# Kernel optimization log

Measured on AMD Instinct MI355X. Metric: run time of the kernel, lower is better.

The kernel has to match this reference:

```python
import jax, jax.numpy as jnp
from jax import lax
import numpy as np

B, T, IN, H, NC = 2048, 512, 1, 128, 8


def setup_inputs() -> dict:
    key = jax.random.key(0)
    ks = jax.random.split(key, 13)
    s = 0.05
    inp = {
        "x": jax.random.normal(ks[0], (B, T, IN), dtype=jnp.float32),
        # layer 0 LSTM params (PyTorch layout: W_ih [4H, in], W_hh [4H, H])
        "W_ih0": jax.random.normal(ks[1], (4 * H, IN), dtype=jnp.float32) * s,
        "W_hh0": jax.random.normal(ks[2], (4 * H, H), dtype=jnp.float32) * s,
        "b_ih0": jax.random.normal(ks[3], (4 * H,), dtype=jnp.float32) * s,
        "b_hh0": jax.random.normal(ks[4], (4 * H,), dtype=jnp.float32) * s,
        # layer 1 LSTM params
        "W_ih1": jax.random.normal(ks[5], (4 * H, H), dtype=jnp.float32) * s,
        "W_hh1": jax.random.normal(ks[6], (4 * H, H), dtype=jnp.float32) * s,
        "b_ih1": jax.random.normal(ks[7], (4 * H,), dtype=jnp.float32) * s,
        "b_hh1": jax.random.normal(ks[8], (4 * H,), dtype=jnp.float32) * s,
        # classifier: Linear(H,64) -> ReLU -> Linear(64,NC)
        "W1": jax.random.normal(ks[9], (64, H), dtype=jnp.float32) * s,
        "b1": jax.random.normal(ks[10], (64,), dtype=jnp.float32) * s,
        "W2": jax.random.normal(ks[11], (NC, 64), dtype=jnp.float32) * s,
        "b2": jax.random.normal(ks[12], (NC,), dtype=jnp.float32) * s,
    }
    return inp


def _lstm_layer(x_seq, W_ih, W_hh, b_ih, b_hh):
    # x_seq: [B, T, in]. PyTorch gate order: i, f, g, o.
    bsz = x_seq.shape[0]
    h_dim = W_hh.shape[1]
    # Precompute input projections for all timesteps (big GEMM outside scan).
    x_proj = jnp.einsum('bti,gi->btg', x_seq, W_ih) + b_ih + b_hh  # [B, T, 4H]

    def step(carry, xp_t):
        h, c = carry
        gates = xp_t + h @ W_hh.T  # [B, 4H]
        i_g, f_g, g_g, o_g = jnp.split(gates, 4, axis=-1)
        i_g = jax.nn.sigmoid(i_g)
        f_g = jax.nn.sigmoid(f_g)
        g_g = jnp.tanh(g_g)
        o_g = jax.nn.sigmoid(o_g)
        c = f_g * c + i_g * g_g
        h = o_g * jnp.tanh(c)
        return (h, c), h

    init = (jnp.zeros((bsz, h_dim), x_seq.dtype), jnp.zeros((bsz, h_dim), x_seq.dtype))
    (_, _), hs = lax.scan(step, init, jnp.swapaxes(x_proj, 0, 1))  # hs: [T, B, H]
    return jnp.swapaxes(hs, 0, 1)  # [B, T, H]


def reference(x, W_ih0, W_hh0, b_ih0, b_hh0, W_ih1, W_hh1, b_ih1, b_hh1, W1, b1, W2, b2):
    h0 = _lstm_layer(x, W_ih0, W_hh0, b_ih0, b_hh0)   # [B, T, H]
    h1 = _lstm_layer(h0, W_ih1, W_hh1, b_ih1, b_hh1)  # [B, T, H] (dropout off in eval)
    last = h1[:, -1, :]                                # [B, H]
    hidden = jax.nn.relu(last @ W1.T + b1)             # [B, 64]
    logits = hidden @ W2.T + b2                        # [B, NC]
    return logits
```

## Files before the change

kernel.cpp:

```cpp
#include <hip/hip_runtime.h>
#include <stdint.h>

typedef float f32x4 __attribute__((ext_vector_type(4)));
typedef short s16x8 __attribute__((ext_vector_type(8)));
typedef short s16x4 __attribute__((ext_vector_type(4)));
typedef uint32_t u32x4 __attribute__((ext_vector_type(4)));

#define HDIM 128
#define TLEN 512
#define BT 16

__device__ __forceinline__ unsigned short f2bf(float f) {
    union { float f; uint32_t u; } v; v.f = f;
    uint32_t r = v.u + 0x7FFFu + ((v.u >> 16) & 1u);
    return (unsigned short)(r >> 16);
}
__device__ __forceinline__ float bfhi(uint32_t u){ union{uint32_t u;float f;}v; v.u = u & 0xFFFF0000u; return v.f; }
__device__ __forceinline__ float bflo(uint32_t u){ union{uint32_t u;float f;}v; v.u = u << 16; return v.f; }
__device__ __forceinline__ float bf2f(short s){ union{uint32_t u;float f;}v; v.u = ((uint32_t)(unsigned short)s) << 16; return v.f; }

__device__ __forceinline__ float sigmoidf_(float x){
    float e = __expf(-x);
    return __builtin_amdgcn_rcpf(1.0f + e);
}
__device__ __forceinline__ float tanhf_(float x){
    float e = __expf(2.0f * x);
    return 1.0f - 2.0f * __builtin_amdgcn_rcpf(1.0f + e);
}

#define MFMA16(A, B, C) __builtin_amdgcn_mfma_f32_16x16x32_bf16((A), (B), (C), 0, 0, 0)

__global__ __launch_bounds__(512, 2) void lstm_fused_kernel(
    const float* __restrict__ x,
    const float* __restrict__ Wih0,
    const float* __restrict__ Whh0,
    const float* __restrict__ bih0,
    const float* __restrict__ bhh0,
    const float* __restrict__ Wih1,
    const float* __restrict__ Whh1,
    const float* __restrict__ bih1,
    const float* __restrict__ bhh1,
    const float* __restrict__ W1,
    const float* __restrict__ b1,
    const float* __restrict__ W2,
    const float* __restrict__ b2,
    float* __restrict__ out)
{
    __shared__ __align__(16) short wh1lds[65536];
    __shared__ __align__(16) short h0f0[2048], h0f1[2048];
    __shared__ __align__(16) short h1f0[2048], h1f1[2048];
    __shared__ __align__(16) float b1lds[4][8][16];

    const int tid = threadIdx.x;
    const int w   = tid >> 6;
    const int wl  = w & 3;
    const bool isL0 = (w < 4);
    const int l = tid & 63;
    const int n = l & 15;
    const int q = l >> 4;
    const int b0 = blockIdx.x * BT;
    const float* xrow = x + (size_t)(b0 + n) * TLEN;

    for (int s2 = tid; s2 < 8192; s2 += 512) {
        const int ll = s2 & 63, t2 = (s2 >> 6) & 7, cc = (s2 >> 9) & 3, wv = s2 >> 11;
        const int row = (t2 >> 1) * 128 + 32 * wv + 16 * (t2 & 1) + (ll & 15);
        const int k0  = cc * 32 + (ll >> 4) * 8;
        const float* p = Whh1 + row * HDIM + k0;
        s16x8 a;
        #pragma unroll
        for (int j = 0; j < 8; ++j) a[j] = (short)f2bf(p[j]);
        *(s16x8*)&wh1lds[s2 * 8] = a;
    }
    {
        const int idx = tid;
        const int wv = idx >> 7, t2 = (idx >> 4) & 7, j = idx & 15;
        const int row = (t2 >> 1) * 128 + 32 * wv + 16 * (t2 & 1) + j;
        b1lds[wv][t2][j] = bih1[row] + bhh1[row];
    }
    for (int s2 = tid; s2 < 1024; s2 += 512) ((uint32_t*)h1f1)[s2] = 0u;

    const int ub0 = 32 * wl + 4 * q;
    const int ub1 = ub0 + 16;
    const int fo0 = ((ub0 >> 5) * 64 + n + 16 * ((ub0 >> 3) & 3)) * 8 + (ub0 & 7);
    const int fo1 = ((ub1 >> 5) * 64 + n + 16 * ((ub1 >> 3) & 3)) * 8 + (ub1 & 7);

#define L0ITER(K, R0, W0) do {                                                \
    const int xi_ = (K) + 1;                                                  \
    const float xv_ = xrow[xi_ < TLEN ? xi_ : (TLEN - 1)];                    \
    s16x8 hb_[4];                                                             \
    _Pragma("unroll")                                                         \
    for (int c = 0; c < 4; ++c) hb_[c] = *(const s16x8*)&(R0)[(c * 64 + l) * 8]; \
    f32x4 a_[8];                                                              \
    _Pragma("unroll")                                                         \
    for (int t2 = 0; t2 < 8; ++t2) {                                          \
        _Pragma("unroll")                                                     \
        for (int r = 0; r < 4; ++r)                                           \
            a_[t2][r] = fmaf(bfhi(bwx[t2][r]), xv_, bflo(bwx[t2][r]));        \
    }                                                                         \
    _Pragma("unroll")                                                         \
    for (int c = 0; c < 4; ++c) {                                             \
        _Pragma("unroll")                                                     \
        for (int t2 = 0; t2 < 8; ++t2)                                        \
            a_[t2] = MFMA16(w0f[c][t2], hb_[c], a_[t2]);                      \
    }                                                                         \
    _Pragma("unroll")                                                         \
    for (int h = 0; h < 2; ++h) {                                             \
        s16x4 hw;                                                             \
        _Pragma("unroll")                                                     \
        for (int r = 0; r < 4; ++r) {                                         \
            const float ig = sigmoidf_(a_[0 + h][r]);                         \
            const float fg = sigmoidf_(a_[2 + h][r]);                         \
            const float gg = tanhf_(a_[4 + h][r]);                            \
            const float og = sigmoidf_(a_[6 + h][r]);                         \
            const float cc = fmaf(fg, c0_[h][r], ig * gg);                    \
            c0_[h][r] = cc;                                                   \
            hw[r] = (short)f2bf(og * tanhf_(cc));                             \
        }                                                                     \
        *(s16x4*)&(W0)[h ? fo1 : fo0] = hw;                                   \
    }                                                                         \
    __syncthreads();                                                          \
} while (0)

#define L1ITER(K, R0, R1, W1) do {                                            \
    s16x8 hb0_[4], hb1_[4];                                                   \
    _Pragma("unroll")                                                         \
    for (int c = 0; c < 4; ++c) {                                             \
        hb0_[c] = *(const s16x8*)&(R0)[(c * 64 + l) * 8];                     \
        hb1_[c] = *(const s16x8*)&(R1)[(c * 64 + l) * 8];                     \
    }                                                                         \
    f32x4 a_[8];                                                              \
    _Pragma("unroll")                                                         \
    for (int t2 = 0; t2 < 8; ++t2)                                            \
        a_[t2] = *(const f32x4*)&b1lds[wl][t2][q * 4];                        \
    _Pragma("unroll")                                                         \
    for (int c = 0; c < 4; ++c) {                                             \
        _Pragma("unroll")                                                     \
        for (int t2 = 0; t2 < 8; ++t2)                                        \
            a_[t2] = MFMA16(wi1f[c][t2], hb0_[c], a_[t2]);                    \
    }                                                                         \
    _Pragma("unroll")                                                         \
    for (int c = 0; c < 4; ++c) {                                             \
        s16x8 wt_[8];                                                         \
        _Pragma("unroll")                                                     \
        for (int t2 = 0; t2 < 8; ++t2)                                        \
            wt_[t2] = *(const s16x8*)&wh1lds[(((wl * 4 + c) * 8 + t2) * 64 + l) * 8]; \
        _Pragma("unroll")                                                     \
        for (int t2 = 0; t2 < 8; ++t2)                                        \
            a_[t2] = MFMA16(wt_[t2], hb1_[c], a_[t2]);                        \
    }                                                                         \
    _Pragma("unroll")                                                         \
    for (int h = 0; h < 2; ++h) {                                             \
        s16x4 hw;                                                             \
        _Pragma("unroll")                                                     \
        for (int r = 0; r < 4; ++r) {                                         \
            const float ig = sigmoidf_(a_[0 + h][r]);                         \
            const float fg = sigmoidf_(a_[2 + h][r]);                         \
            const float gg = tanhf_(a_[4 + h][r]);                            \
            const float og = sigmoidf_(a_[6 + h][r]);                         \
            const float cc = fmaf(fg, c1_[h][r], ig * gg);                    \
            c1_[h][r] = cc;                                                   \
            hw[r] = (short)f2bf(og * tanhf_(cc));                             \
        }                                                                     \
        *(s16x4*)&(W1)[h ? fo1 : fo0] = hw;                                   \
    }                                                                         \
    __syncthreads();                                                          \
} while (0)

    if (isL0) {
        s16x8 w0f[4][8];
        #pragma unroll
        for (int c = 0; c < 4; ++c) {
            #pragma unroll
            for (int t2 = 0; t2 < 8; ++t2) {
                const int row = (t2 >> 1) * 128 + 32 * wl + 16 * (t2 & 1) + n;
                const int k0 = c * 32 + q * 8;
                const float* p = Whh0 + row * HDIM + k0;
                s16x8 a;
                #pragma unroll
                for (int j = 0; j < 8; ++j) a[j] = (short)f2bf(p[j]);
                w0f[c][t2] = a;
            }
        }
        u32x4 bwx[8];
        #pragma unroll
        for (int t2 = 0; t2 < 8; ++t2) {
            #pragma unroll
            for (int r = 0; r < 4; ++r) {
                const int row = (t2 >> 1) * 128 + 32 * wl + 16 * (t2 & 1) + 4 * q + r;
                bwx[t2][r] = ((uint32_t)f2bf(Wih0[row]) << 16) | f2bf(bih0[row] + bhh0[row]);
            }
        }
        float c0_[2][4] = {{0.f,0.f,0.f,0.f},{0.f,0.f,0.f,0.f}};

        {
            const float x0 = xrow[0];
            #pragma unroll
            for (int h = 0; h < 2; ++h) {
                s16x4 hw;
                #pragma unroll
                for (int r = 0; r < 4; ++r) {
                    const float pi = fmaf(bfhi(bwx[0 + h][r]), x0, bflo(bwx[0 + h][r]));
                    const float pg = fmaf(bfhi(bwx[4 + h][r]), x0, bflo(bwx[4 + h][r]));
                    const float po = fmaf(bfhi(bwx[6 + h][r]), x0, bflo(bwx[6 + h][r]));
                    const float ig = sigmoidf_(pi);
                    const float gg = tanhf_(pg);
                    const float og = sigmoidf_(po);
                    const float cc = ig * gg;
                    c0_[h][r] = cc;
                    hw[r] = (short)f2bf(og * tanhf_(cc));
                }
                *(s16x4*)&h0f0[h ? fo1 : fo0] = hw;
            }
        }
        __syncthreads();

        #pragma unroll 1
        for (int k = 0; k < TLEN; k += 2) {
            L0ITER(k,     h0f0, h0f1);
            L0ITER(k + 1, h0f1, h0f0);
        }
    } else {
        s16x8 wi1f[4][8];
        #pragma unroll
        for (int c = 0; c < 4; ++c) {
            #pragma unroll
            for (int t2 = 0; t2 < 8; ++t2) {
                const int row = (t2 >> 1) * 128 + 32 * wl + 16 * (t2 & 1) + n;
                const int k0 = c * 32 + q * 8;
                const float* p = Wih1 + row * HDIM + k0;
                s16x8 a;
                #pragma unroll
                for (int j = 0; j < 8; ++j) a[j] = (short)f2bf(p[j]);
                wi1f[c][t2] = a;
            }
        }
        float c1_[2][4] = {{0.f,0.f,0.f,0.f},{0.f,0.f,0.f,0.f}};

        __syncthreads();

        #pragma unroll 1
        for (int k = 0; k < TLEN; k += 2) {
            L1ITER(k,     h0f0, h1f1, h1f0);
            L1ITER(k + 1, h0f1, h1f0, h1f1);
        }
    }

    float* headH = (float*)wh1lds;
    float* headL = headH + 16 * HDIM;
    if (!isL0) {
        #pragma unroll
        for (int h = 0; h < 2; ++h) {
            const s16x4 hv = *(const s16x4*)&h1f1[h ? fo1 : fo0];
            f32x4 hf;
            #pragma unroll
            for (int r = 0; r < 4; ++r) hf[r] = bf2f(hv[r]);
            *(f32x4*)&headH[n * HDIM + (h ? ub1 : ub0)] = hf;
        }
    }
    __syncthreads();

    #pragma unroll
    for (int rep = 0; rep < 2; ++rep) {
        const int idx = tid + rep * 512;
        const int nn = idx >> 6, j = idx & 63;
        float s = b1[j];
        const float* wrow = W1 + j * HDIM;
        const float* hrow = headH + nn * HDIM;
        #pragma unroll
        for (int k = 0; k < HDIM; k += 4) {
            const f32x4 hv = *(const f32x4*)&hrow[k];
            const f32x4 wv = *(const f32x4*)&wrow[k];
            s += hv[0]*wv[0] + hv[1]*wv[1] + hv[2]*wv[2] + hv[3]*wv[3];
        }
        headL[nn * 64 + j] = fmaxf(s, 0.0f);
    }
    __syncthreads();

    if (tid < 128) {
        const int nn = tid >> 3, cls = tid & 7;
        float s = b2[cls];
        const float* wrow = W2 + cls * 64;
        const float* hrow = headL + nn * 64;
        #pragma unroll
        for (int k = 0; k < 64; k += 4) {
            const f32x4 hv = *(const f32x4*)&hrow[k];
            const f32x4 wv = *(const f32x4*)&wrow[k];
            s += hv[0]*wv[0] + hv[1]*wv[1] + hv[2]*wv[2] + hv[3]*wv[3];
        }
        out[(size_t)(b0 + nn) * 8 + cls] = s;
    }
}

extern "C" void kernel_launch(void* const* d_in, const int* in_sizes, int n_in,
                              void* d_out, int out_size, void* d_ws, size_t ws_size,
                              hipStream_t stream) {
    const float* x    = (const float*)d_in[0];
    const float* Wih0 = (const float*)d_in[1];
    const float* Whh0 = (const float*)d_in[2];
    const float* bih0 = (const float*)d_in[3];
    const float* bhh0 = (const float*)d_in[4];
    const float* Wih1 = (const float*)d_in[5];
    const float* Whh1 = (const float*)d_in[6];
    const float* bih1 = (const float*)d_in[7];
    const float* bhh1 = (const float*)d_in[8];
    const float* W1   = (const float*)d_in[9];
    const float* b1   = (const float*)d_in[10];
    const float* W2   = (const float*)d_in[11];
    const float* b2   = (const float*)d_in[12];
    float* outp = (float*)d_out;

    lstm_fused_kernel<<<128, 512, 0, stream>>>(
        x, Wih0, Whh0, bih0, bhh0, Wih1, Whh1, bih1, bhh1, W1, b1, W2, b2, outp);
}
```

Before: 954.4 us.

## Replace block barriers with LDS counter flags and 4-deep h0 ring buffer

The per-timestep __syncthreads between layer-0 and layer-1 wavegroups is replaced by LDS atomic counters that each wave polls with s_sleep. A 4-slot ring buffer for layer-0 hidden states lets layer 0 run up to two steps ahead of layer 1, so the two layers no longer stall in lockstep. The last layer-1 step is peeled out and writes fp32 h directly to the head buffer. The cost is spin-wait polling overhead and fragile memory-ordering assumptions around the LDS flags.

```diff
diff --git a/kernel.cpp b/kernel.cpp
--- a/kernel.cpp
+++ b/kernel.cpp
@@ -47,9 +47,10 @@
     float* __restrict__ out)
 {
     __shared__ __align__(16) short wh1lds[65536];
-    __shared__ __align__(16) short h0f0[2048], h0f1[2048];
-    __shared__ __align__(16) short h1f0[2048], h1f1[2048];
+    __shared__ __align__(16) short h0ring[4][2048];
+    __shared__ __align__(16) short h1f[2][2048];
     __shared__ __align__(16) float b1lds[4][8][16];
+    __shared__ int syncc[2];
 
     const int tid = threadIdx.x;
     const int w   = tid >> 6;
@@ -61,6 +62,8 @@
     const int b0 = blockIdx.x * BT;
     const float* xrow = x + (size_t)(b0 + n) * TLEN;
 
+    if (tid == 0) { syncc[0] = 0; syncc[1] = 0; }
+
     for (int s2 = tid; s2 < 8192; s2 += 512) {
         const int ll = s2 & 63, t2 = (s2 >> 6) & 7, cc = (s2 >> 9) & 3, wv = s2 >> 11;
         const int row = (t2 >> 1) * 128 + 32 * wv + 16 * (t2 & 1) + (ll & 15);
@@ -77,93 +80,23 @@
         const int row = (t2 >> 1) * 128 + 32 * wv + 16 * (t2 & 1) + j;
         b1lds[wv][t2][j] = bih1[row] + bhh1[row];
     }
-    for (int s2 = tid; s2 < 1024; s2 += 512) ((uint32_t*)h1f1)[s2] = 0u;
+    for (int s2 = tid; s2 < 1024; s2 += 512) ((uint32_t*)h1f[1])[s2] = 0u;
 
     const int ub0 = 32 * wl + 4 * q;
     const int ub1 = ub0 + 16;
     const int fo0 = ((ub0 >> 5) * 64 + n + 16 * ((ub0 >> 3) & 3)) * 8 + (ub0 & 7);
     const int fo1 = ((ub1 >> 5) * 64 + n + 16 * ((ub1 >> 3) & 3)) * 8 + (ub1 & 7);
 
-#define L0ITER(K, R0, W0) do {                                                \
-    const int xi_ = (K) + 1;                                                  \
-    const float xv_ = xrow[xi_ < TLEN ? xi_ : (TLEN - 1)];                    \
-    s16x8 hb_[4];                                                             \
-    _Pragma("unroll")                                                         \
-    for (int c = 0; c < 4; ++c) hb_[c] = *(const s16x8*)&(R0)[(c * 64 + l) * 8]; \
-    f32x4 a_[8];                                                              \
-    _Pragma("unroll")                                                         \
-    for (int t2 = 0; t2 < 8; ++t2) {                                          \
-        _Pragma("unroll")                                                     \
-        for (int r = 0; r < 4; ++r)                                           \
-            a_[t2][r] = fmaf(bfhi(bwx[t2][r]), xv_, bflo(bwx[t2][r]));        \
-    }                                                                         \
-    _Pragma("unroll")                                                         \
-    for (int c = 0; c < 4; ++c) {                                             \
-        _Pragma("unroll")                                                     \
-        for (int t2 = 0; t2 < 8; ++t2)                                        \
-            a_[t2] = MFMA16(w0f[c][t2], hb_[c], a_[t2]);                      \
-    }                                                                         \
-    _Pragma("unroll")                                                         \
-    for (int h = 0; h < 2; ++h) {                                             \
-        s16x4 hw;                                                             \
-        _Pragma("unroll")                                                     \
-        for (int r = 0; r < 4; ++r) {                                         \
-            const float ig = sigmoidf_(a_[0 + h][r]);                         \
-            const float fg = sigmoidf_(a_[2 + h][r]);                         \
-            const float gg = tanhf_(a_[4 + h][r]);                            \
-            const float og = sigmoidf_(a_[6 + h][r]);                         \
-            const float cc = fmaf(fg, c0_[h][r], ig * gg);                    \
-            c0_[h][r] = cc;                                                   \
-            hw[r] = (short)f2bf(og * tanhf_(cc));                             \
-        }                                                                     \
-        *(s16x4*)&(W0)[h ? fo1 : fo0] = hw;                                   \
-    }                                                                         \
-    __syncthreads();                                                          \
+#define WAITGE(T0, T1) do {                                                   \
+    volatile const int* f0_ = &syncc[0];                                      \
+    volatile const int* f1_ = &syncc[1];                                      \
+    while (*f0_ < (T0) || *f1_ < (T1)) __builtin_amdgcn_s_sleep(1);           \
+    __threadfence_block();                                                    \
 } while (0)
 
-#define L1ITER(K, R0, R1, W1) do {                                            \
-    s16x8 hb0_[4], hb1_[4];                                                   \
-    _Pragma("unroll")                                                         \
-    for (int c = 0; c < 4; ++c) {                                             \
-        hb0_[c] = *(const s16x8*)&(R0)[(c * 64 + l) * 8];                     \
-        hb1_[c] = *(const s16x8*)&(R1)[(c * 64 + l) * 8];                     \
-    }                                                                         \
-    f32x4 a_[8];                                                              \
-    _Pragma("unroll")                                                         \
-    for (int t2 = 0; t2 < 8; ++t2)                                            \
-        a_[t2] = *(const f32x4*)&b1lds[wl][t2][q * 4];                        \
-    _Pragma("unroll")                                                         \
-    for (int c = 0; c < 4; ++c) {                                             \
-        _Pragma("unroll")                                                     \
-        for (int t2 = 0; t2 < 8; ++t2)                                        \
-            a_[t2] = MFMA16(wi1f[c][t2], hb0_[c], a_[t2]);                    \
-    }                                                                         \
-    _Pragma("unroll")                                                         \
-    for (int c = 0; c < 4; ++c) {                                             \
-        s16x8 wt_[8];                                                         \
-        _Pragma("unroll")                                                     \
-        for (int t2 = 0; t2 < 8; ++t2)                                        \
-            wt_[t2] = *(const s16x8*)&wh1lds[(((wl * 4 + c) * 8 + t2) * 64 + l) * 8]; \
-        _Pragma("unroll")                                                     \
-        for (int t2 = 0; t2 < 8; ++t2)                                        \
-            a_[t2] = MFMA16(wt_[t2], hb1_[c], a_[t2]);                        \
-    }                                                                         \
-    _Pragma("unroll")                                                         \
-    for (int h = 0; h < 2; ++h) {                                             \
-        s16x4 hw;                                                             \
-        _Pragma("unroll")                                                     \
-        for (int r = 0; r < 4; ++r) {                                         \
-            const float ig = sigmoidf_(a_[0 + h][r]);                         \
-            const float fg = sigmoidf_(a_[2 + h][r]);                         \
-            const float gg = tanhf_(a_[4 + h][r]);                            \
-            const float og = sigmoidf_(a_[6 + h][r]);                         \
-            const float cc = fmaf(fg, c1_[h][r], ig * gg);                    \
-            c1_[h][r] = cc;                                                   \
-            hw[r] = (short)f2bf(og * tanhf_(cc));                             \
-        }                                                                     \
-        *(s16x4*)&(W1)[h ? fo1 : fo0] = hw;                                   \
-    }                                                                         \
-    __syncthreads();                                                          \
+#define POST(TM) do {                                                         \
+    __threadfence_block();                                                    \
+    if (l == 0) atomicAdd(&syncc[TM], 1);                                     \
 } while (0)
 
     if (isL0) {
@@ -209,15 +142,49 @@
                     c0_[h][r] = cc;
                     hw[r] = (short)f2bf(og * tanhf_(cc));
                 }
-                *(s16x4*)&h0f0[h ? fo1 : fo0] = hw;
+                *(s16x4*)&h0ring[0][h ? fo1 : fo0] = hw;
             }
         }
         __syncthreads();
 
         #pragma unroll 1
-        for (int k = 0; k < TLEN; k += 2) {
-            L0ITER(k,     h0f0, h0f1);
-            L0ITER(k + 1, h0f1, h0f0);
+        for (int i = 0; i < 511; ++i) {
+            WAITGE(4 * i, 4 * (i - 2));
+            const short* R0 = h0ring[i & 3];
+            short*       W0 = h0ring[(i + 1) & 3];
+            const float xv_ = xrow[i + 1];
+            s16x8 hb_[4];
+            #pragma unroll
+            for (int c = 0; c < 4; ++c) hb_[c] = *(const s16x8*)&R0[(c * 64 + l) * 8];
+            f32x4 a_[8];
+            #pragma unroll
+            for (int t2 = 0; t2 < 8; ++t2) {
+                #pragma unroll
+                for (int r = 0; r < 4; ++r)
+                    a_[t2][r] = fmaf(bfhi(bwx[t2][r]), xv_, bflo(bwx[t2][r]));
+            }
+            #pragma unroll
+            for (int c = 0; c < 4; ++c) {
+                #pragma unroll
+                for (int t2 = 0; t2 < 8; ++t2)
+                    a_[t2] = MFMA16(w0f[c][t2], hb_[c], a_[t2]);
+            }
+            #pragma unroll
+            for (int h = 0; h < 2; ++h) {
+                s16x4 hw;
+                #pragma unroll
+                for (int r = 0; r < 4; ++r) {
+                    const float ig = sigmoidf_(a_[0 + h][r]);
+                    const float fg = sigmoidf_(a_[2 + h][r]);
+                    const float gg = tanhf_(a_[4 + h][r]);
+                    const float og = sigmoidf_(a_[6 + h][r]);
+                    const float cc = fmaf(fg, c0_[h][r], ig * gg);
+                    c0_[h][r] = cc;
+                    hw[r] = (short)f2bf(og * tanhf_(cc));
+                }
+                *(s16x4*)&W0[h ? fo1 : fo0] = hw;
+            }
+            POST(0);
         }
     } else {
         s16x8 wi1f[4][8];
@@ -239,25 +206,103 @@
         __syncthreads();
 
         #pragma unroll 1
-        for (int k = 0; k < TLEN; k += 2) {
-            L1ITER(k,     h0f0, h1f1, h1f0);
-            L1ITER(k + 1, h0f1, h1f0, h1f1);
-        }
-    }
-
-    float* headH = (float*)wh1lds;
-    float* headL = headH + 16 * HDIM;
-    if (!isL0) {
-        #pragma unroll
-        for (int h = 0; h < 2; ++h) {
-            const s16x4 hv = *(const s16x4*)&h1f1[h ? fo1 : fo0];
-            f32x4 hf;
-            #pragma unroll
-            for (int r = 0; r < 4; ++r) hf[r] = bf2f(hv[r]);
-            *(f32x4*)&headH[n * HDIM + (h ? ub1 : ub0)] = hf;
-        }
-    }
+        for (int k = 0; k < 511; ++k) {
+            WAITGE(4 * k, 4 * k);
+            const short* R0 = h0ring[k & 3];
+            const short* R1 = h1f[(k + 1) & 1];
+            short*       W1B = h1f[k & 1];
+            s16x8 hb0_[4], hb1_[4];
+            #pragma unroll
+            for (int c = 0; c < 4; ++c) {
+                hb0_[c] = *(const s16x8*)&R0[(c * 64 + l) * 8];
+                hb1_[c] = *(const s16x8*)&R1[(c * 64 + l) * 8];
+            }
+            f32x4 a_[8];
+            #pragma unroll
+            for (int t2 = 0; t2 < 8; ++t2)
+                a_[t2] = *(const f32x4*)&b1lds[wl][t2][q * 4];
+            #pragma unroll
+            for (int c = 0; c < 4; ++c) {
+                #pragma unroll
+                for (int t2 = 0; t2 < 8; ++t2)
+                    a_[t2] = MFMA16(wi1f[c][t2], hb0_[c], a_[t2]);
+            }
+            #pragma unroll
+            for (int c = 0; c < 4; ++c) {
+                s16x8 wt_[8];
+                #pragma unroll
+                for (int t2 = 0; t2 < 8; ++t2)
+                    wt_[t2] = *(const s16x8*)&wh1lds[(((wl * 4 + c) * 8 + t2) * 64 + l) * 8];
+                #pragma unroll
+                for (int t2 = 0; t2 < 8; ++t2)
+                    a_[t2] = MFMA16(wt_[t2], hb1_[c], a_[t2]);
+            }
+            #pragma unroll
+            for (int h = 0; h < 2; ++h) {
+                s16x4 hw;
+                #pragma unroll
+                for (int r = 0; r < 4; ++r) {
+                    const float ig = sigmoidf_(a_[0 + h][r]);
+                    const float fg = sigmoidf_(a_[2 + h][r]);
+                    const float gg = tanhf_(a_[4 + h][r]);
+                    const float og = sigmoidf_(a_[6 + h][r]);
+                    const float cc = fmaf(fg, c1_[h][r], ig * gg);
+                    c1_[h][r] = cc;
+                    hw[r] = (short)f2bf(og * tanhf_(cc));
+                }
+                *(s16x4*)&W1B[h ? fo1 : fo0] = hw;
+            }
+            POST(1);
+        }
+
+        WAITGE(4 * 511, 4 * 511);
+        {
+            const short* R0 = h0ring[511 & 3];
+            const short* R1 = h1f[0];
+            s16x8 hb0_[4], hb1_[4];
+            #pragma unroll
+            for (int c = 0; c < 4; ++c) {
+                hb0_[c] = *(const s16x8*)&R0[(c * 64 + l) * 8];
+                hb1_[c] = *(const s16x8*)&R1[(c * 64 + l) * 8];
+            }
+            f32x4 a_[8];
+            #pragma unroll
+            for (int t2 = 0; t2 < 8; ++t2)
+                a_[t2] = *(const f32x4*)&b1lds[wl][t2][q * 4];
+            #pragma unroll
+            for (int c = 0; c < 4; ++c) {
+                s16x8 wt_[8];
+                #pragma unroll
+                for (int t2 = 0; t2 < 8; ++t2)
+                    wt_[t2] = *(const s16x8*)&wh1lds[(((wl * 4 + c) * 8 + t2) * 64 + l) * 8];
+                #pragma unroll
+                for (int t2 = 0; t2 < 8; ++t2) {
+                    a_[t2] = MFMA16(wi1f[c][t2], hb0_[c], a_[t2]);
+                    a_[t2] = MFMA16(wt_[t2], hb1_[c], a_[t2]);
+                }
+            }
+            float* headH = (float*)&h0ring[0][0];
+            #pragma unroll
+            for (int h = 0; h < 2; ++h) {
+                f32x4 hv;
+                #pragma unroll
+                for (int r = 0; r < 4; ++r) {
+                    const float ig = sigmoidf_(a_[0 + h][r]);
+                    const float fg = sigmoidf_(a_[2 + h][r]);
+                    const float gg = tanhf_(a_[4 + h][r]);
+                    const float og = sigmoidf_(a_[6 + h][r]);
+                    const float cc = fmaf(fg, c1_[h][r], ig * gg);
+                    hv[r] = og * tanhf_(cc);
+                }
+                *(f32x4*)&headH[n * HDIM + (h ? ub1 : ub0)] = hv;
+            }
+        }
+    }
+
     __syncthreads();
+
+    float* headH = (float*)&h0ring[0][0];
+    float* headL = (float*)&h1f[0][0];
 
     #pragma unroll
     for (int rep = 0; rep < 2; ++rep) {
```

New measurement: 1.095 ms. +14.7%, slower.

## Split LSTM layers across paired workgroups with global ring buffer and flags

Applied to the files above, without the earlier changes.

Adds a pipelined kernel in which each batch tile gets two workgroups: one runs layer 0 and streams each step's hidden state into a global ring buffer, publishing progress flags every 8 steps. The other runs layer 1, spin-waits on those flags and prefetches the next layer-0 state while it computes. Both layers' weights stay in registers, and the grid doubles to 256 blocks to use more CUs. The new path needs a large workspace (about 256 MB) and a memset, otherwise it falls back to the old kernel. It also relies on both blocks of a pair being co-resident and adds global-memory traffic plus flag polling latency.

```diff
diff --git a/kernel.cpp b/kernel.cpp
--- a/kernel.cpp
+++ b/kernel.cpp
@@ -29,6 +29,318 @@
 }
 
 #define MFMA16(A, B, C) __builtin_amdgcn_mfma_f32_16x16x32_bf16((A), (B), (C), 0, 0, 0)
+#define UNPK(arr, idx) (((idx) & 1) ? bfhi(arr[(idx) >> 1]) : bflo(arr[(idx) >> 1]))
+
+__global__ __launch_bounds__(512, 2) void lstm_pipe_kernel(
+    const float* __restrict__ x,
+    const float* __restrict__ Wih0,
+    const float* __restrict__ Whh0,
+    const float* __restrict__ bih0,
+    const float* __restrict__ bhh0,
+    const float* __restrict__ Wih1,
+    const float* __restrict__ Whh1,
+    const float* __restrict__ bih1,
+    const float* __restrict__ bhh1,
+    const float* __restrict__ W1,
+    const float* __restrict__ b1,
+    const float* __restrict__ W2,
+    const float* __restrict__ b2,
+    short* __restrict__ ring,
+    int* __restrict__ flags,
+    float* __restrict__ out)
+{
+    __shared__ __align__(16) short h0A[2][2048];
+    __shared__ __align__(16) short h1f[2][2048];
+    __shared__ __align__(16) float headH[16 * HDIM];
+    __shared__ __align__(16) float headL[16 * 64];
+
+    const int role = blockIdx.x & 1;
+    const int p    = blockIdx.x >> 1;
+    const int tid  = threadIdx.x;
+    const int w = tid >> 6;
+    const int l = tid & 63;
+    const int n = l & 15;
+    const int q = l >> 4;
+    const int b0 = p * BT;
+    const float* xrow = x + (size_t)(b0 + n) * TLEN;
+    short* ringp = ring + (size_t)p * TLEN * 2048;
+
+    const int u0 = w * 16 + q * 4;
+    const int fragoff = (((u0 >> 5) * 64) + n + 16 * ((u0 >> 3) & 3)) * 8 + (u0 & 7);
+
+    if (role == 0) {
+        s16x8 w0f[4][4];
+        #pragma unroll
+        for (int c = 0; c < 4; ++c) {
+            #pragma unroll
+            for (int tile = 0; tile < 4; ++tile) {
+                const int g  = tile * 128 + w * 16 + n;
+                const int k0 = c * 32 + q * 8;
+                const float* pw = Whh0 + g * HDIM + k0;
+                s16x8 a;
+                #pragma unroll
+                for (int j = 0; j < 8; ++j) a[j] = (short)f2bf(pw[j]);
+                w0f[c][tile] = a;
+            }
+        }
+        uint32_t b0p[8], wxp[8];
+        #pragma unroll
+        for (int i = 0; i < 8; ++i) {
+            const int tr0 = 2 * i;
+            const int tile = tr0 >> 2, r0 = tr0 & 3;
+            const int g0 = tile * 128 + u0 + r0;
+            const int g1 = g0 + 1;
+            b0p[i] = ((uint32_t)f2bf(bih0[g1] + bhh0[g1]) << 16) | f2bf(bih0[g0] + bhh0[g0]);
+            wxp[i] = ((uint32_t)f2bf(Wih0[g1]) << 16) | f2bf(Wih0[g0]);
+        }
+        float c0v[4] = {0.f, 0.f, 0.f, 0.f};
+
+        {
+            const float x0 = xrow[0];
+            s16x4 hw;
+            #pragma unroll
+            for (int r = 0; r < 4; ++r) {
+                const float pi = fmaf(UNPK(wxp, r),      x0, UNPK(b0p, r));
+                const float pg = fmaf(UNPK(wxp, 8 + r),  x0, UNPK(b0p, 8 + r));
+                const float po = fmaf(UNPK(wxp, 12 + r), x0, UNPK(b0p, 12 + r));
+                const float ig = sigmoidf_(pi);
+                const float gg = tanhf_(pg);
+                const float og = sigmoidf_(po);
+                const float cc = ig * gg;
+                c0v[r] = cc;
+                hw[r] = (short)f2bf(og * tanhf_(cc));
+            }
+            *(s16x4*)&h0A[0][fragoff] = hw;
+            *(s16x4*)&ringp[fragoff] = hw;
+        }
+        __syncthreads();
+
+        #pragma unroll 1
+        for (int i = 0; i < 511; ++i) {
+            const short* R = h0A[i & 1];
+            short*       W = h0A[(i + 1) & 1];
+            const float xv = xrow[i + 1];
+            s16x8 hb[4];
+            #pragma unroll
+            for (int c = 0; c < 4; ++c) hb[c] = *(const s16x8*)&R[(c * 64 + l) * 8];
+            f32x4 a[4];
+            #pragma unroll
+            for (int tile = 0; tile < 4; ++tile) {
+                #pragma unroll
+                for (int r = 0; r < 4; ++r) {
+                    const int tr = tile * 4 + r;
+                    a[tile][r] = fmaf(UNPK(wxp, tr), xv, UNPK(b0p, tr));
+                }
+            }
+            #pragma unroll
+            for (int c = 0; c < 4; ++c) {
+                #pragma unroll
+                for (int tile = 0; tile < 4; ++tile)
+                    a[tile] = MFMA16(w0f[c][tile], hb[c], a[tile]);
+            }
+            s16x4 hw;
+            #pragma unroll
+            for (int r = 0; r < 4; ++r) {
+                const float ig = sigmoidf_(a[0][r]);
+                const float fg = sigmoidf_(a[1][r]);
+                const float gg = tanhf_(a[2][r]);
+                const float og = sigmoidf_(a[3][r]);
+                const float cc = fmaf(fg, c0v[r], ig * gg);
+                c0v[r] = cc;
+                hw[r] = (short)f2bf(og * tanhf_(cc));
+            }
+            *(s16x4*)&W[fragoff] = hw;
+            *(s16x4*)&ringp[(size_t)(i + 1) * 2048 + fragoff] = hw;
+
+            if (((i + 2) & 7) == 0) {
+                __threadfence();
+                __syncthreads();
+                if (tid == 0)
+                    __hip_atomic_store(&flags[p], (i + 2) >> 3,
+                                       __ATOMIC_RELEASE, __HIP_MEMORY_SCOPE_AGENT);
+            } else {
+                __syncthreads();
+            }
+        }
+        return;
+    }
+
+    s16x8 wi1f[4][4], wh1f[4][4];
+    #pragma unroll
+    for (int c = 0; c < 4; ++c) {
+        #pragma unroll
+        for (int tile = 0; tile < 4; ++tile) {
+            const int g  = tile * 128 + w * 16 + n;
+            const int k0 = c * 32 + q * 8;
+            const float* p1 = Wih1 + g * HDIM + k0;
+            const float* p2 = Whh1 + g * HDIM + k0;
+            s16x8 a, b;
+            #pragma unroll
+            for (int j = 0; j < 8; ++j) { a[j] = (short)f2bf(p1[j]); b[j] = (short)f2bf(p2[j]); }
+            wi1f[c][tile] = a; wh1f[c][tile] = b;
+        }
+    }
+    uint32_t b1p[8];
+    #pragma unroll
+    for (int i = 0; i < 8; ++i) {
+        const int tr0 = 2 * i;
+        const int tile = tr0 >> 2, r0 = tr0 & 3;
+        const int g0 = tile * 128 + u0 + r0;
+        const int g1 = g0 + 1;
+        b1p[i] = ((uint32_t)f2bf(bih1[g1] + bhh1[g1]) << 16) | f2bf(bih1[g0] + bhh1[g0]);
+    }
+    for (int s2 = tid; s2 < 1024; s2 += 512) ((uint32_t*)h1f[1])[s2] = 0u;
+    float c1v[4] = {0.f, 0.f, 0.f, 0.f};
+
+#define WAITCHUNK(C) do {                                                     \
+    if (tid == 0) {                                                           \
+        while (__hip_atomic_load(&flags[p], __ATOMIC_ACQUIRE,                 \
+                                 __HIP_MEMORY_SCOPE_AGENT) < (C))             \
+            __builtin_amdgcn_s_sleep(8);                                      \
+    }                                                                         \
+    __syncthreads();                                                          \
+    __threadfence();         \
+} while (0)
+
+#define LOADCUR(DST, T) do {                                                  \
+    _Pragma("unroll")                                                         \
+    for (int c = 0; c < 4; ++c)                                               \
+        (DST)[c] = *(const s16x8*)&ringp[(size_t)(T) * 2048 + (c * 64 + l) * 8]; \
+} while (0)
+
+#define BSTEP(K, CUR, NXT, DO_PF) do {                                        \
+    const short* R1_ = h1f[((K) + 1) & 1];                                    \
+    short*       W1_ = h1f[(K) & 1];                                          \
+    s16x8 hb1_[4];                                                            \
+    _Pragma("unroll")                                                         \
+    for (int c = 0; c < 4; ++c) hb1_[c] = *(const s16x8*)&R1_[(c * 64 + l) * 8]; \
+    f32x4 a_[4];                                                              \
+    _Pragma("unroll")                                                         \
+    for (int tile = 0; tile < 4; ++tile) {                                    \
+        _Pragma("unroll")                                                     \
+        for (int r = 0; r < 4; ++r) a_[tile][r] = UNPK(b1p, tile * 4 + r);    \
+    }                                                                         \
+    _Pragma("unroll")                                                         \
+    for (int c = 0; c < 4; ++c) {                                             \
+        _Pragma("unroll")                                                     \
+        for (int tile = 0; tile < 4; ++tile)                                  \
+            a_[tile] = MFMA16(wi1f[c][tile], (CUR)[c], a_[tile]);             \
+    }                                                                         \
+    if (DO_PF) { LOADCUR(NXT, (K) + 1); }                                     \
+    _Pragma("unroll")                                                         \
+    for (int c = 0; c < 4; ++c) {                                             \
+        _Pragma("unroll")                                                     \
+        for (int tile = 0; tile < 4; ++tile)                                  \
+            a_[tile] = MFMA16(wh1f[c][tile], hb1_[c], a_[tile]);              \
+    }                                                                         \
+    s16x4 hw_;                                                                \
+    _Pragma("unroll")                                                         \
+    for (int r = 0; r < 4; ++r) {                                             \
+        const float ig = sigmoidf_(a_[0][r]);                                 \
+        const float fg = sigmoidf_(a_[1][r]);                                 \
+        const float gg = tanhf_(a_[2][r]);                                    \
+        const float og = sigmoidf_(a_[3][r]);                                 \
+        const float cc = fmaf(fg, c1v[r], ig * gg);                           \
+        c1v[r] = cc;                                                          \
+        hw_[r] = (short)f2bf(og * tanhf_(cc));                                \
+    }                                                                         \
+    *(s16x4*)&W1_[fragoff] = hw_;                                             \
+    __syncthreads();                                                          \
+} while (0)
+
+    s16x8 curA[4], curB[4];
+
+    #pragma unroll 1
+    for (int c64 = 0; c64 < 63; ++c64) {
+        WAITCHUNK(c64 + 1);
+        const int kb = 8 * c64;
+        LOADCUR(curA, kb);
+        BSTEP(kb + 0, curA, curB, true);
+        BSTEP(kb + 1, curB, curA, true);
+        BSTEP(kb + 2, curA, curB, true);
+        BSTEP(kb + 3, curB, curA, true);
+        BSTEP(kb + 4, curA, curB, true);
+        BSTEP(kb + 5, curB, curA, true);
+        BSTEP(kb + 6, curA, curB, true);
+        BSTEP(kb + 7, curB, curA, false);
+    }
+    WAITCHUNK(64);
+    LOADCUR(curA, 504);
+    BSTEP(504, curA, curB, true);
+    BSTEP(505, curB, curA, true);
+    BSTEP(506, curA, curB, true);
+    BSTEP(507, curB, curA, true);
+    BSTEP(508, curA, curB, true);
+    BSTEP(509, curB, curA, true);
+    BSTEP(510, curA, curB, true);
+
+    {
+        const short* R1 = h1f[0];
+        s16x8 hb1_[4];
+        #pragma unroll
+        for (int c = 0; c < 4; ++c) hb1_[c] = *(const s16x8*)&R1[(c * 64 + l) * 8];
+        f32x4 a_[4];
+        #pragma unroll
+        for (int tile = 0; tile < 4; ++tile) {
+            #pragma unroll
+            for (int r = 0; r < 4; ++r) a_[tile][r] = UNPK(b1p, tile * 4 + r);
+        }
+        #pragma unroll
+        for (int c = 0; c < 4; ++c) {
+            #pragma unroll
+            for (int tile = 0; tile < 4; ++tile) {
+                a_[tile] = MFMA16(wi1f[c][tile], curB[c], a_[tile]);
+                a_[tile] = MFMA16(wh1f[c][tile], hb1_[c], a_[tile]);
+            }
+        }
+        f32x4 hv;
+        #pragma unroll
+        for (int r = 0; r < 4; ++r) {
+            const float ig = sigmoidf_(a_[0][r]);
+            const float fg = sigmoidf_(a_[1][r]);
+            const float gg = tanhf_(a_[2][r]);
+            const float og = sigmoidf_(a_[3][r]);
+            const float cc = fmaf(fg, c1v[r], ig * gg);
+            hv[r] = og * tanhf_(cc);
+        }
+        *(f32x4*)&headH[n * HDIM + u0] = hv;
+    }
+    __syncthreads();
+
+    #pragma unroll
+    for (int rep = 0; rep < 2; ++rep) {
+        const int idx = tid + rep * 512;
+        const int nn = idx >> 6, j = idx & 63;
+        float s = b1[j];
+        const float* wrow = W1 + j * HDIM;
+        const float* hrow = headH + nn * HDIM;
+        #pragma unroll
+        for (int k = 0; k < HDIM; k += 4) {
+            const f32x4 hv = *(const f32x4*)&hrow[k];
+            const f32x4 wv = *(const f32x4*)&wrow[k];
+            s += hv[0]*wv[0] + hv[1]*wv[1] + hv[2]*wv[2] + hv[3]*wv[3];
+        }
+        headL[nn * 64 + j] = fmaxf(s, 0.0f);
+    }
+    __syncthreads();
+
+    if (tid < 128) {
+        const int nn = tid >> 3, cls = tid & 7;
+        float s = b2[cls];
+        const float* wrow = W2 + cls * 64;
+        const float* hrow = headL + nn * 64;
+        #pragma unroll
+        for (int k = 0; k < 64; k += 4) {
+            const f32x4 hv = *(const f32x4*)&hrow[k];
+            const f32x4 wv = *(const f32x4*)&wrow[k];
+            s += hv[0]*wv[0] + hv[1]*wv[1] + hv[2]*wv[2] + hv[3]*wv[3];
+        }
+        out[(size_t)(b0 + nn) * 8 + cls] = s;
+    }
+#undef WAITCHUNK
+#undef LOADCUR
+#undef BSTEP
+}
 
 __global__ __launch_bounds__(512, 2) void lstm_fused_kernel(
     const float* __restrict__ x,
@@ -191,7 +503,6 @@
             }
         }
         float c0_[2][4] = {{0.f,0.f,0.f,0.f},{0.f,0.f,0.f,0.f}};
-
         {
             const float x0 = xrow[0];
             #pragma unroll
@@ -213,7 +524,6 @@
             }
         }
         __syncthreads();
-
         #pragma unroll 1
         for (int k = 0; k < TLEN; k += 2) {
             L0ITER(k,     h0f0, h0f1);
@@ -235,15 +545,20 @@
             }
         }
         float c1_[2][4] = {{0.f,0.f,0.f,0.f},{0.f,0.f,0.f,0.f}};
-
         __syncthreads();
-
         #pragma unroll 1
         for (int k = 0; k < TLEN; k += 2) {
             L1ITER(k,     h0f0, h1f1, h1f0);
             L1ITER(k + 1, h0f1, h1f0, h1f1);
         }
-    }
+        {
+            const short* R0 = h0f0;
+            const short* R1 = h1f1;
+            (void)R0; (void)R1;
+        }
+    }
+
+    __syncthreads();
 
     float* headH = (float*)wh1lds;
     float* headL = headH + 16 * HDIM;
@@ -289,6 +604,8 @@
         }
         out[(size_t)(b0 + nn) * 8 + cls] = s;
     }
+#undef L0ITER
+#undef L1ITER
 }
 
 extern "C" void kernel_launch(void* const* d_in, const int* in_sizes, int n_in,
@@ -309,6 +626,19 @@
     const float* b2   = (const float*)d_in[12];
     float* outp = (float*)d_out;
 
-    lstm_fused_kernel<<<128, 512, 0, stream>>>(
-        x, Wih0, Whh0, bih0, bhh0, Wih1, Whh1, bih1, bhh1, W1, b1, W2, b2, outp);
+    const size_t ring_bytes = (size_t)128 * TLEN * 2048 * sizeof(short);
+    const size_t need = 4096 + ring_bytes;
+
+    if (ws_size >= need) {
+        int*   flags = (int*)d_ws;
+        short* ring  = (short*)((char*)d_ws + 4096);
+        hipMemsetAsync(d_ws, 0, 4096, stream);
+        lstm_pipe_kernel<<<256, 512, 0, stream>>>(
+            x, Wih0, Whh0, bih0, bhh0, Wih1, Whh1, bih1, bhh1,
+            W1, b1, W2, b2, ring, flags, outp);
+    } else {
+        lstm_fused_kernel<<<128, 512, 0, stream>>>(
+            x, Wih0, Whh0, bih0, bhh0, Wih1, Whh1, bih1, bhh1,
+            W1, b1, W2, b2, outp);
+    }
 }
```

Result: no change. 954.8 us (+0.0%).

## Add 1024-thread LSTM kernel with global-cached packed W_ih1 and per-layer warps

Applied to the files above, without the earlier changes.

Adds a new fused kernel using 1024 threads per block: 8 warps run layer 0 and 8 warps run layer 1. Each warp now owns 16 hidden units instead of 32, so per-wave register pressure drops and each step has twice as many waves in flight. W_hh1 is packed into LDS. W_ih1 is pre-packed into bf16 MFMA fragment order by a separate kernel into workspace and streamed from global/L2 each step. This trades register residency for per-step global loads plus an extra launch. The old kernel is kept as a fallback when the workspace is too small.

```diff
diff --git a/kernel.cpp b/kernel.cpp
--- a/kernel.cpp
+++ b/kernel.cpp
@@ -29,6 +29,266 @@
 }
 
 #define MFMA16(A, B, C) __builtin_amdgcn_mfma_f32_16x16x32_bf16((A), (B), (C), 0, 0, 0)
+
+__global__ __launch_bounds__(1024) void pack_wih1_kernel(
+    const float* __restrict__ Wih1, short* __restrict__ dst)
+{
+    const int s2 = blockIdx.x * 1024 + threadIdx.x;
+    const int ll = s2 & 63;
+    const int t  = (s2 >> 6) & 3;
+    const int c  = (s2 >> 8) & 3;
+    const int wl = s2 >> 10;
+    const float* p = Wih1 + (t * 128 + wl * 16 + (ll & 15)) * HDIM + c * 32 + (ll >> 4) * 8;
+    s16x8 a;
+    #pragma unroll
+    for (int j = 0; j < 8; ++j) a[j] = (short)f2bf(p[j]);
+    *(s16x8*)&dst[s2 * 8] = a;
+}
+
+__global__ __launch_bounds__(1024, 4) void lstm_mega_kernel(
+    const float* __restrict__ x,
+    const float* __restrict__ Wih0,
+    const float* __restrict__ Whh0,
+    const float* __restrict__ bih0,
+    const float* __restrict__ bhh0,
+    const float* __restrict__ Whh1,
+    const float* __restrict__ bih1,
+    const float* __restrict__ bhh1,
+    const float* __restrict__ W1,
+    const float* __restrict__ b1,
+    const float* __restrict__ W2,
+    const float* __restrict__ b2,
+    const short* __restrict__ wih1pk,
+    float* __restrict__ out)
+{
+    __shared__ __align__(16) short whh1lds[65536];
+    __shared__ __align__(16) short h0f[2][2048];
+    __shared__ __align__(16) short h1f[2][2048];
+    __shared__ __align__(16) uint32_t b0wx[8][4][16];
+    __shared__ __align__(16) float    b1t[8][4][16];
+
+    const int tid = threadIdx.x;
+    const int w   = tid >> 6;
+    const int wl  = w & 7;
+    const bool isL0 = (w < 8);
+    const int l = tid & 63;
+    const int n = l & 15;
+    const int q = l >> 4;
+    const int b0 = blockIdx.x * BT;
+    const float* xrow = x + (size_t)(b0 + n) * TLEN;
+
+    #pragma unroll
+    for (int i = 0; i < 8; ++i) {
+        const int s2 = tid + i * 1024;
+        const int ll = s2 & 63, t = (s2 >> 6) & 3, c = (s2 >> 8) & 3, wv = s2 >> 10;
+        const float* p = Whh1 + (t * 128 + wv * 16 + (ll & 15)) * HDIM + c * 32 + (ll >> 4) * 8;
+        s16x8 a;
+        #pragma unroll
+        for (int j = 0; j < 8; ++j) a[j] = (short)f2bf(p[j]);
+        *(s16x8*)&whh1lds[s2 * 8] = a;
+    }
+    if (tid < 512) {
+        const int wv = tid >> 6, t = (tid >> 4) & 3, j = tid & 15;
+        const int row = t * 128 + wv * 16 + j;
+        b0wx[wv][t][j] = ((uint32_t)f2bf(Wih0[row]) << 16) | f2bf(bih0[row] + bhh0[row]);
+    } else {
+        const int idx = tid - 512;
+        const int wv = idx >> 6, t = (idx >> 4) & 3, j = idx & 15;
+        const int row = t * 128 + wv * 16 + j;
+        b1t[wv][t][j] = bih1[row] + bhh1[row];
+    }
+    ((uint32_t*)h1f[1])[tid] = 0u;
+
+    const int u0 = wl * 16 + q * 4;
+    const int fragoff = ((u0 >> 5) * 64 + n + 16 * ((u0 >> 3) & 3)) * 8 + (u0 & 7);
+
+#define L0ITER(K, R, W) do {                                                  \
+    const int xi_ = (K) + 1;                                                  \
+    const float xv_ = xrow[xi_ < TLEN ? xi_ : (TLEN - 1)];                    \
+    s16x8 hb_[4];                                                             \
+    _Pragma("unroll")                                                         \
+    for (int c = 0; c < 4; ++c) hb_[c] = *(const s16x8*)&(R)[(c * 64 + l) * 8]; \
+    f32x4 acc_[4];                                                            \
+    _Pragma("unroll")                                                         \
+    for (int t = 0; t < 4; ++t) {                                             \
+        const u32x4 bwt = *(const u32x4*)&b0wx[wl][t][q * 4];                 \
+        _Pragma("unroll")                                                     \
+        for (int r = 0; r < 4; ++r)                                           \
+            acc_[t][r] = fmaf(bfhi(bwt[r]), xv_, bflo(bwt[r]));               \
+    }                                                                         \
+    _Pragma("unroll")                                                         \
+    for (int c = 0; c < 4; ++c) {                                             \
+        _Pragma("unroll")                                                     \
+        for (int t = 0; t < 4; ++t)                                           \
+            acc_[t] = MFMA16(w0f[c][t], hb_[c], acc_[t]);                     \
+    }                                                                         \
+    s16x4 hw_;                                                                \
+    _Pragma("unroll")                                                         \
+    for (int r = 0; r < 4; ++r) {                                             \
+        const float ig = sigmoidf_(acc_[0][r]);                               \
+        const float fg = sigmoidf_(acc_[1][r]);                               \
+        const float gg = tanhf_(acc_[2][r]);                                  \
+        const float og = sigmoidf_(acc_[3][r]);                               \
+        const float cc = fmaf(fg, c0v[r], ig * gg);                           \
+        c0v[r] = cc;                                                          \
+        hw_[r] = (short)f2bf(og * tanhf_(cc));                                \
+    }                                                                         \
+    *(s16x4*)&(W)[fragoff] = hw_;                                             \
+    __syncthreads();                                                          \
+} while (0)
+
+#define LOADWI(DST, C) do {                                                   \
+    _Pragma("unroll")                                                         \
+    for (int t4 = 0; t4 < 4; ++t4)                                            \
+        (DST)[t4] = *(const s16x8*)&wih1pk[(((wl * 4 + (C)) * 4 + t4) * 64 + l) * 8]; \
+} while (0)
+
+#define L1ITER(K, R0, R1, W1B) do {                                           \
+    s16x8 wiA_[4], wiB_[4];                                                   \
+    LOADWI(wiA_, 0); LOADWI(wiB_, 1);                                         \
+    s16x8 hb0_[4], hb1_[4];                                                   \
+    _Pragma("unroll")                                                         \
+    for (int c = 0; c < 4; ++c) {                                             \
+        hb0_[c] = *(const s16x8*)&(R0)[(c * 64 + l) * 8];                     \
+        hb1_[c] = *(const s16x8*)&(R1)[(c * 64 + l) * 8];                     \
+    }                                                                         \
+    f32x4 acc_[4];                                                            \
+    _Pragma("unroll")                                                         \
+    for (int t = 0; t < 4; ++t) acc_[t] = *(const f32x4*)&b1t[wl][t][q * 4];  \
+    _Pragma("unroll")                                                         \
+    for (int c = 0; c < 4; ++c) {                                             \
+        s16x8 wt_[4];                                                         \
+        _Pragma("unroll")                                                     \
+        for (int t = 0; t < 4; ++t)                                           \
+            wt_[t] = *(const s16x8*)&whh1lds[(((wl * 4 + c) * 4 + t) * 64 + l) * 8]; \
+        _Pragma("unroll")                                                     \
+        for (int t = 0; t < 4; ++t)                                           \
+            acc_[t] = MFMA16(wt_[t], hb1_[c], acc_[t]);                       \
+    }                                                                         \
+    _Pragma("unroll")                                                         \
+    for (int t = 0; t < 4; ++t) acc_[t] = MFMA16(wiA_[t], hb0_[0], acc_[t]);  \
+    LOADWI(wiA_, 2);                                                          \
+    _Pragma("unroll")                                                         \
+    for (int t = 0; t < 4; ++t) acc_[t] = MFMA16(wiB_[t], hb0_[1], acc_[t]);  \
+    LOADWI(wiB_, 3);                                                          \
+    _Pragma("unroll")                                                         \
+    for (int t = 0; t < 4; ++t) acc_[t] = MFMA16(wiA_[t], hb0_[2], acc_[t]);  \
+    _Pragma("unroll")                                                         \
+    for (int t = 0; t < 4; ++t) acc_[t] = MFMA16(wiB_[t], hb0_[3], acc_[t]);  \
+    s16x4 hw_;                                                                \
+    _Pragma("unroll")                                                         \
+    for (int r = 0; r < 4; ++r) {                                             \
+        const float ig = sigmoidf_(acc_[0][r]);                               \
+        const float fg = sigmoidf_(acc_[1][r]);                               \
+        const float gg = tanhf_(acc_[2][r]);                                  \
+        const float og = sigmoidf_(acc_[3][r]);                               \
+        const float cc = fmaf(fg, c1v[r], ig * gg);                           \
+        c1v[r] = cc;                                                          \
+        hw_[r] = (short)f2bf(og * tanhf_(cc));                                \
+    }                                                                         \
+    *(s16x4*)&(W1B)[fragoff] = hw_;                                           \
+    __syncthreads();                                                          \
+} while (0)
+
+    if (isL0) {
+        s16x8 w0f[4][4];
+        #pragma unroll
+        for (int c = 0; c < 4; ++c) {
+            #pragma unroll
+            for (int t = 0; t < 4; ++t) {
+                const float* p = Whh0 + (t * 128 + wl * 16 + n) * HDIM + c * 32 + q * 8;
+                s16x8 a;
+                #pragma unroll
+                for (int j = 0; j < 8; ++j) a[j] = (short)f2bf(p[j]);
+                w0f[c][t] = a;
+            }
+        }
+        float c0v[4] = {0.f, 0.f, 0.f, 0.f};
+
+        __syncthreads();
+
+        {
+            const float x0 = xrow[0];
+            u32x4 bw0 = *(const u32x4*)&b0wx[wl][0][q * 4];
+            u32x4 bw2 = *(const u32x4*)&b0wx[wl][2][q * 4];
+            u32x4 bw3 = *(const u32x4*)&b0wx[wl][3][q * 4];
+            s16x4 hw;
+            #pragma unroll
+            for (int r = 0; r < 4; ++r) {
+                const float pi = fmaf(bfhi(bw0[r]), x0, bflo(bw0[r]));
+                const float pg = fmaf(bfhi(bw2[r]), x0, bflo(bw2[r]));
+                const float po = fmaf(bfhi(bw3[r]), x0, bflo(bw3[r]));
+                const float ig = sigmoidf_(pi);
+                const float gg = tanhf_(pg);
+                const float og = sigmoidf_(po);
+                const float cc = ig * gg;
+                c0v[r] = cc;
+                hw[r] = (short)f2bf(og * tanhf_(cc));
+            }
+            *(s16x4*)&h0f[0][fragoff] = hw;
+        }
+        __syncthreads();
+
+        #pragma unroll 1
+        for (int k = 0; k < TLEN; k += 2) {
+            L0ITER(k,     h0f[0], h0f[1]);
+            L0ITER(k + 1, h0f[1], h0f[0]);
+        }
+    } else {
+        float c1v[4] = {0.f, 0.f, 0.f, 0.f};
+        __syncthreads();
+        __syncthreads();
+
+        #pragma unroll 1
+        for (int k = 0; k < TLEN; k += 2) {
+            L1ITER(k,     h0f[0], h1f[1], h1f[0]);
+            L1ITER(k + 1, h0f[1], h1f[0], h1f[1]);
+        }
+    }
+
+    float* headH = (float*)whh1lds;
+    float* headL = headH + 16 * HDIM;
+    if (!isL0) {
+        const s16x4 hv = *(const s16x4*)&h1f[1][fragoff];
+        f32x4 hf;
+        #pragma unroll
+        for (int r = 0; r < 4; ++r) hf[r] = bf2f(hv[r]);
+        *(f32x4*)&headH[n * HDIM + u0] = hf;
+    }
+    __syncthreads();
+
+    {
+        const int nn = tid >> 6, j = tid & 63;
+        float s = b1[j];
+        const float* wrow = W1 + j * HDIM;
+        const float* hrow = headH + nn * HDIM;
+        #pragma unroll
+        for (int k = 0; k < HDIM; k += 4) {
+            const f32x4 hv = *(const f32x4*)&hrow[k];
+            const f32x4 wv = *(const f32x4*)&wrow[k];
+            s += hv[0]*wv[0] + hv[1]*wv[1] + hv[2]*wv[2] + hv[3]*wv[3];
+        }
+        headL[nn * 64 + j] = fmaxf(s, 0.0f);
+    }
+    __syncthreads();
+
+    if (tid < 128) {
+        const int nn = tid >> 3, cls = tid & 7;
+        float s = b2[cls];
+        const float* wrow = W2 + cls * 64;
+        const float* hrow = headL + nn * 64;
+        #pragma unroll
+        for (int k = 0; k < 64; k += 4) {
+            const f32x4 hv = *(const f32x4*)&hrow[k];
+            const f32x4 wv = *(const f32x4*)&wrow[k];
+            s += hv[0]*wv[0] + hv[1]*wv[1] + hv[2]*wv[2] + hv[3]*wv[3];
+        }
+        out[(size_t)(b0 + nn) * 8 + cls] = s;
+    }
+#undef L0ITER
+#undef LOADWI
+#undef L1ITER
+}
 
 __global__ __launch_bounds__(512, 2) void lstm_fused_kernel(
     const float* __restrict__ x,
@@ -191,7 +451,6 @@
             }
         }
         float c0_[2][4] = {{0.f,0.f,0.f,0.f},{0.f,0.f,0.f,0.f}};
-
         {
             const float x0 = xrow[0];
             #pragma unroll
@@ -213,7 +472,6 @@
             }
         }
         __syncthreads();
-
         #pragma unroll 1
         for (int k = 0; k < TLEN; k += 2) {
             L0ITER(k,     h0f0, h0f1);
@@ -235,15 +493,15 @@
             }
         }
         float c1_[2][4] = {{0.f,0.f,0.f,0.f},{0.f,0.f,0.f,0.f}};
-
         __syncthreads();
-
         #pragma unroll 1
         for (int k = 0; k < TLEN; k += 2) {
             L1ITER(k,     h0f0, h1f1, h1f0);
             L1ITER(k + 1, h0f1, h1f0, h1f1);
         }
     }
+
+    __syncthreads();
 
     float* headH = (float*)wh1lds;
     float* headL = headH + 16 * HDIM;
@@ -289,6 +547,8 @@
         }
         out[(size_t)(b0 + nn) * 8 + cls] = s;
     }
+#undef L0ITER
+#undef L1ITER
 }
 
 extern "C" void kernel_launch(void* const* d_in, const int* in_sizes, int n_in,
@@ -309,6 +569,17 @@
     const float* b2   = (const float*)d_in[12];
     float* outp = (float*)d_out;
 
-    lstm_fused_kernel<<<128, 512, 0, stream>>>(
-        x, Wih0, Whh0, bih0, bhh0, Wih1, Whh1, bih1, bhh1, W1, b1, W2, b2, outp);
-}
+    const size_t PACK_BYTES = (size_t)512 * 128 * sizeof(short);
+
+    if (ws_size >= PACK_BYTES) {
+        short* wih1pk = (short*)d_ws;
+        pack_wih1_kernel<<<8, 1024, 0, stream>>>(Wih1, wih1pk);
+        lstm_mega_kernel<<<128, 1024, 0, stream>>>(
+            x, Wih0, Whh0, bih0, bhh0, Whh1, bih1, bhh1,
+            W1, b1, W2, b2, wih1pk, outp);
+    } else {
+        lstm_fused_kernel<<<128, 512, 0, stream>>>(
+            x, Wih0, Whh0, bih0, bhh0, Wih1, Whh1, bih1, bhh1,
+            W1, b1, W2, b2, outp);
+    }
+}
```

Measured after the change: 889.6 us, median of 2. -6.8%, faster.
